# Kernel optimization log

Measured on AMD Instinct MI355X. Metric: run time of the kernel, lower is better.

## Reference

```python
import jax, jax.numpy as jnp
import numpy as np

GRID_SIZE = 128  # D = H = W
N_POINTS = 8388608


def setup_inputs() -> dict:
    key = jax.random.key(0)
    k_grid, k_coords = jax.random.split(key)
    # occupancy grid buffer: binary {0,1} values as float, shape [D, H, W]
    grid = (jax.random.uniform(k_grid, (GRID_SIZE, GRID_SIZE, GRID_SIZE)) > 0.5).astype(jnp.float32)
    # normalized [-1, 1] query coordinates, layout [..., 3] = (x, y, z)
    coords = jax.random.uniform(k_coords, (N_POINTS, 3), minval=-1.0, maxval=1.0, dtype=jnp.float32)
    return {"grid": grid, "coords": coords}


def _trilinear_sample(grid, coords):
    """torch.nn.functional.grid_sample 5D, mode='bilinear', align_corners=False,
    padding_mode='zeros'. grid: [D,H,W]; coords: [N,3] with (x,y,z) where
    x indexes W, y indexes H, z indexes D. Returns [N]."""
    D, H, W = grid.shape
    x, y, z = coords[:, 0], coords[:, 1], coords[:, 2]
    # unnormalize (align_corners=False): pixel = ((c + 1) * size - 1) / 2
    ix = ((x + 1.0) * W - 1.0) * 0.5
    iy = ((y + 1.0) * H - 1.0) * 0.5
    iz = ((z + 1.0) * D - 1.0) * 0.5

    ix0 = jnp.floor(ix)
    iy0 = jnp.floor(iy)
    iz0 = jnp.floor(iz)
    wx = ix - ix0  # fractional weights
    wy = iy - iy0
    wz = iz - iz0
    ix0 = ix0.astype(jnp.int32)
    iy0 = iy0.astype(jnp.int32)
    iz0 = iz0.astype(jnp.int32)

    def gather(zi, yi, xi):
        # zero padding: out-of-bounds corners contribute 0
        valid = ((zi >= 0) & (zi < D) & (yi >= 0) & (yi < H) & (xi >= 0) & (xi < W))
        zc = jnp.clip(zi, 0, D - 1)
        yc = jnp.clip(yi, 0, H - 1)
        xc = jnp.clip(xi, 0, W - 1)
        return jnp.where(valid, grid[zc, yc, xc], 0.0)

    out = (
        gather(iz0,     iy0,     ix0    ) * (1 - wz) * (1 - wy) * (1 - wx)
        + gather(iz0,     iy0,     ix0 + 1) * (1 - wz) * (1 - wy) * wx
        + gather(iz0,     iy0 + 1, ix0    ) * (1 - wz) * wy       * (1 - wx)
        + gather(iz0,     iy0 + 1, ix0 + 1) * (1 - wz) * wy       * wx
        + gather(iz0 + 1, iy0,     ix0    ) * wz       * (1 - wy) * (1 - wx)
        + gather(iz0 + 1, iy0,     ix0 + 1) * wz       * (1 - wy) * wx
        + gather(iz0 + 1, iy0 + 1, ix0    ) * wz       * wy       * (1 - wx)
        + gather(iz0 + 1, iy0 + 1, ix0 + 1) * wz       * wy       * wx
    )
    return out


def reference(grid, coords):
    flat = coords.reshape(-1, 3)
    return _trilinear_sample(grid, flat)
```

## Files before the change

kernel.cpp:

```cpp
#include <hip/hip_runtime.h>


typedef float fx4 __attribute__((ext_vector_type(4)));
typedef unsigned int u32;
typedef unsigned int ux4 __attribute__((ext_vector_type(4)));
typedef unsigned long long u64;

constexpr int GS = 128;
constexpr int PROW_W  = 5;
constexpr int PPLANE_W = 130 * PROW_W;
constexpr int PMASK_WORDS = 130 * PPLANE_W;
constexpr size_t PMASK_BYTES = (size_t)PMASK_WORDS * 4;

constexpr size_t MASK_BYTES = (size_t)GS * GS * GS / 8;
constexpr size_t MASK_OFF   = (PMASK_BYTES + 63) & ~(size_t)63;
constexpr size_t WS_MAIN    = MASK_OFF + MASK_BYTES;

constexpr int TD = GS + 1;
constexpr size_t TBL_BYTES = (size_t)TD * TD * TD;
constexpr size_t TBL_OFF   = MASK_OFF + MASK_BYTES;
constexpr size_t WS_FB     = TBL_OFF + TBL_BYTES;

constexpr int SLAB_ALLOC_WORDS = 46 * PPLANE_W + 1;
constexpr size_t SLAB_LDS = (size_t)SLAB_ALLOC_WORDS * 4;

__global__ __launch_bounds__(256)
void bitpack_kernel(const float* __restrict__ grid, u64* __restrict__ mask) {
    int gid = blockIdx.x * blockDim.x + threadIdx.x;
    float v = grid[gid];
    u64 m = __ballot(v != 0.0f);
    if ((threadIdx.x & 63) == 0) mask[gid >> 6] = m;
}

__global__ __launch_bounds__(256)
void padmask_kernel(const u32* __restrict__ mask32, u32* __restrict__ pmask) {
    int i = blockIdx.x * blockDim.x + threadIdx.x;
    if (i >= PMASK_WORDS) return;
    int k = i % PROW_W;
    int r = i / PROW_W;
    int py = r % 130;
    int pz = r / 130;
    int y = py - 1, z = pz - 1;
    u32 w = 0;
    if (((unsigned)y < 128u) & ((unsigned)z < 128u)) {
        const u32* vrow = mask32 + (z * 128 + y) * 4;
        u32 lo = (k >= 1) ? vrow[k - 1] : 0u;
        u32 hi = (k < 4) ? vrow[k] : 0u;
        w = (lo >> 31) | (hi << 1);
    }
    pmask[i] = w;
}

__global__ __launch_bounds__(1024, 4)
void sample_slab3(const u32* __restrict__ pmask,
                  const float* __restrict__ coords,
                  float* __restrict__ out) {
    extern __shared__ u32 lds[];
    const int tid = threadIdx.x;
    const int T = blockIdx.x * 1024 + tid;
    const fx4* c4 = (const fx4*)coords;
    fx4 q[6];
#pragma unroll
    for (int j = 0; j < 6; ++j) q[j] = c4[6 * T + j];
    const float* f = (const float*)q;

    u32 pr[8];
    float wx[8], wy[8], wz[8], o[8];
#pragma unroll
    for (int j = 0; j < 8; ++j) {
        float ix = fmaf(f[3 * j + 0], 64.0f, 63.5f);
        float iy = fmaf(f[3 * j + 1], 64.0f, 63.5f);
        float iz = fmaf(f[3 * j + 2], 64.0f, 63.5f);
        float fx = floorf(ix), fy = floorf(iy), fz = floorf(iz);
        wx[j] = ix - fx; wy[j] = iy - fy; wz[j] = iz - fz;
        int X  = (int)fx + 1;
        int Y  = (int)fy + 1;
        int PZ = (int)fz + 1;
        int k = X >> 5, p = X & 31;
        u32 R = (u32)((PZ * 130 + Y) * PROW_W + k);
        pr[j] = R | ((u32)p << 20) | ((u32)PZ << 25);
        o[j] = 0.0f;
    }

#pragma unroll 1
    for (int s = 0; s < 3; ++s) {
        const int p0 = (s == 0) ? 0 : (s == 1 ? 44 : 88);
        const int np = (s == 2) ? 42 : 46;
        const int lo = (s == 0) ? 0 : (s == 1 ? 45 : 89);
        const int hi = (s == 0) ? 44 : (s == 1 ? 88 : 128);
        __syncthreads();
        {
            const int nv = np * PPLANE_W / 4;
            const ux4* src = (const ux4*)(pmask + p0 * PPLANE_W);
            ux4* dst = (ux4*)lds;
            for (int i = tid; i < nv; i += 1024) dst[i] = src[i];
        }
        __syncthreads();
#pragma unroll
        for (int j = 0; j < 8; ++j) {
            int PZ = (int)(pr[j] >> 25);
            if ((unsigned)(PZ - lo) > (unsigned)(hi - lo)) continue;
            int p  = (int)((pr[j] >> 20) & 31u);
            int rb = (int)(pr[j] & 0xFFFFFu) - p0 * PPLANE_W;
            int rb2 = rb + PPLANE_W;
            u32 a0 = lds[rb],      a1 = lds[rb + 1];
            u32 b0 = lds[rb + 5],  b1 = lds[rb + 6];
            u32 c0 = lds[rb2],     c1 = lds[rb2 + 1];
            u32 d0 = lds[rb2 + 5], d1 = lds[rb2 + 6];
            u32 t00 = (u32)((((u64)a1 << 32) | a0) >> p) & 3u;
            u32 t01 = (u32)((((u64)b1 << 32) | b0) >> p) & 3u;
            u32 t10 = (u32)((((u64)c1 << 32) | c0) >> p) & 3u;
            u32 t11 = (u32)((((u64)d1 << 32) | d0) >> p) & 3u;
            float w = wx[j];
            float r00 = fmaf(w, (float)(t00 >> 1) - (float)(t00 & 1u), (float)(t00 & 1u));
            float r01 = fmaf(w, (float)(t01 >> 1) - (float)(t01 & 1u), (float)(t01 & 1u));
            float r10 = fmaf(w, (float)(t10 >> 1) - (float)(t10 & 1u), (float)(t10 & 1u));
            float r11 = fmaf(w, (float)(t11 >> 1) - (float)(t11 & 1u), (float)(t11 & 1u));
            float cy0 = fmaf(wy[j], r01 - r00, r00);
            float cy1 = fmaf(wy[j], r11 - r10, r10);
            o[j] = fmaf(wz[j], cy1 - cy0, cy0);
        }
    }
    fx4* o4 = (fx4*)out;
    fx4 r0 = {o[0], o[1], o[2], o[3]};
    fx4 r1 = {o[4], o[5], o[6], o[7]};
    o4[2 * T]     = r0;
    o4[2 * T + 1] = r1;
}

__device__ __forceinline__ unsigned bit_at(u64 lo, u64 hi, int xi) {
    if ((unsigned)xi >= 128u) return 0u;
    u64 w = (xi < 64) ? lo : hi;
    return (unsigned)((w >> (xi & 63)) & 1ull);
}

__global__ __launch_bounds__(256)
void table_kernel(const u64* __restrict__ mask, unsigned char* __restrict__ tbl) {
    int i = blockIdx.x * blockDim.x + threadIdx.x;
    if (i >= (int)TBL_BYTES) return;
    int x = i % TD;
    int t = i / TD;
    int y = t % TD;
    int z = t / TD;
    int x0 = x - 1;
    unsigned byte = 0u;
#pragma unroll
    for (int dz = 0; dz < 2; ++dz) {
#pragma unroll
        for (int dy = 0; dy < 2; ++dy) {
            int yi = y - 1 + dy, zi = z - 1 + dz;
            u64 lo = 0ull, hi = 0ull;
            if (((unsigned)yi < 128u) & ((unsigned)zi < 128u)) {
                int r = (zi * 128 + yi) * 2;
                lo = mask[r];
                hi = mask[r + 1];
            }
            int kk = dy * 2 + dz * 4;
            byte |= (bit_at(lo, hi, x0) << kk) | (bit_at(lo, hi, x0 + 1) << (kk + 1));
        }
    }
    tbl[i] = (unsigned char)byte;
}

__global__ __launch_bounds__(256)
void sample_packed(const unsigned char* __restrict__ tbl,
                   const float* __restrict__ coords,
                   float* __restrict__ out, int nt) {
    int t = blockIdx.x * blockDim.x + threadIdx.x;
    if (t >= nt) return;
    const fx4* c4 = (const fx4*)coords;
    fx4 q[6];
#pragma unroll
    for (int j = 0; j < 6; ++j) q[j] = c4[6 * t + j];
    const float* f = (const float*)q;
    float wxa[8], wya[8], wza[8];
    int addr[8];
#pragma unroll
    for (int i = 0; i < 8; ++i) {
        float ix = fmaf(f[3 * i + 0], 64.0f, 63.5f);
        float iy = fmaf(f[3 * i + 1], 64.0f, 63.5f);
        float iz = fmaf(f[3 * i + 2], 64.0f, 63.5f);
        float fx = floorf(ix), fy = floorf(iy), fz = floorf(iz);
        wxa[i] = ix - fx; wya[i] = iy - fy; wza[i] = iz - fz;
        int xb = (int)fx + 1, yb = (int)fy + 1, zb = (int)fz + 1;
        addr[i] = (zb * TD + yb) * TD + xb;
    }
    unsigned bytes[8];
#pragma unroll
    for (int i = 0; i < 8; ++i) bytes[i] = (unsigned)tbl[addr[i]];
    float o[8];
#pragma unroll
    for (int i = 0; i < 8; ++i) {
        unsigned byte = bytes[i];
        float wx = wxa[i], wy = wya[i], wz = wza[i];
        float v0 = (float)( byte       & 1u);
        float v1 = (float)((byte >> 1) & 1u);
        float v2 = (float)((byte >> 2) & 1u);
        float v3 = (float)((byte >> 3) & 1u);
        float v4 = (float)((byte >> 4) & 1u);
        float v5 = (float)((byte >> 5) & 1u);
        float v6 = (float)((byte >> 6) & 1u);
        float v7 = (float)((byte >> 7) & 1u);
        float c00 = v0 + wx * (v1 - v0);
        float c10 = v2 + wx * (v3 - v2);
        float c01 = v4 + wx * (v5 - v4);
        float c11 = v6 + wx * (v7 - v6);
        float c0  = c00 + wy * (c10 - c00);
        float c1  = c01 + wy * (c11 - c01);
        o[i] = c0 + wz * (c1 - c0);
    }
    fx4* o4 = (fx4*)out;
    fx4 r0 = {o[0], o[1], o[2], o[3]};
    fx4 r1 = {o[4], o[5], o[6], o[7]};
    o4[2 * t + 0] = r0;
    o4[2 * t + 1] = r1;
}

extern "C" void kernel_launch(void* const* d_in, const int* in_sizes, int n_in,
                              void* d_out, int out_size, void* d_ws, size_t ws_size,
                              hipStream_t stream) {
    const float* grid   = (const float*)d_in[0];
    const float* coords = (const float*)d_in[1];
    float* out = (float*)d_out;
    int npts = in_sizes[1] / 3;
    int vox = GS * GS * GS;

    u32* pmask = (u32*)d_ws;
    u64* mask  = (u64*)((char*)d_ws + MASK_OFF);

    (void)hipFuncSetAttribute((const void*)sample_slab3,
                              hipFuncAttributeMaxDynamicSharedMemorySize,
                              (int)SLAB_LDS);
    int nb = 0;
    hipError_t oe = hipOccupancyMaxActiveBlocksPerMultiprocessor(
        &nb, sample_slab3, 1024, SLAB_LDS);
    bool slab_ok = (oe == hipSuccess) && (nb >= 1) && (ws_size >= WS_MAIN) &&
                   (npts == 1024 * 1024 * 8);

    if (slab_ok) {
        bitpack_kernel<<<vox / 256, 256, 0, stream>>>(grid, mask);
        padmask_kernel<<<(PMASK_WORDS + 255) / 256, 256, 0, stream>>>((const u32*)mask, pmask);
        sample_slab3<<<1024, 1024, SLAB_LDS, stream>>>(pmask, coords, out);
    } else if (ws_size >= WS_FB) {
        unsigned char* tbl = (unsigned char*)d_ws + TBL_OFF;
        bitpack_kernel<<<vox / 256, 256, 0, stream>>>(grid, mask);
        table_kernel<<<(int)((TBL_BYTES + 255) / 256), 256, 0, stream>>>(mask, tbl);
        int nt = npts / 8;
        sample_packed<<<(nt + 255) / 256, 256, 0, stream>>>(tbl, coords, out, nt);
    }
}
```

Before: 194.7 us.

## Sample from unpadded bitmask in two LDS slabs, dropping padmask kernel

Removes the padded-mask kernel and samples directly from the raw 128^3 bitmask. The grid is now staged into LDS in two z-slabs of about 130KB each instead of three padded slabs. Out-of-bounds corners are handled with per-point validity masks, an x-flip trick at the left edge, and alignbit for the bit extraction. This cuts one kernel launch, one slab pass and its barriers, in exchange for more per-point mask arithmetic and more LDS per block, which may lower occupancy.

```diff
diff --git a/kernel.cpp b/kernel.cpp
--- a/kernel.cpp
+++ b/kernel.cpp
@@ -7,22 +7,14 @@
 typedef unsigned long long u64;
 
 constexpr int GS = 128;
-constexpr int PROW_W  = 5;
-constexpr int PPLANE_W = 130 * PROW_W;
-constexpr int PMASK_WORDS = 130 * PPLANE_W;
-constexpr size_t PMASK_BYTES = (size_t)PMASK_WORDS * 4;
-
 constexpr size_t MASK_BYTES = (size_t)GS * GS * GS / 8;
-constexpr size_t MASK_OFF   = (PMASK_BYTES + 63) & ~(size_t)63;
-constexpr size_t WS_MAIN    = MASK_OFF + MASK_BYTES;
+constexpr int SLAB_WORDS = 33281;
+constexpr size_t SLAB_LDS = (size_t)SLAB_WORDS * 4;
 
 constexpr int TD = GS + 1;
 constexpr size_t TBL_BYTES = (size_t)TD * TD * TD;
-constexpr size_t TBL_OFF   = MASK_OFF + MASK_BYTES;
+constexpr size_t TBL_OFF   = (MASK_BYTES + 63) & ~(size_t)63;
 constexpr size_t WS_FB     = TBL_OFF + TBL_BYTES;
-
-constexpr int SLAB_ALLOC_WORDS = 46 * PPLANE_W + 1;
-constexpr size_t SLAB_LDS = (size_t)SLAB_ALLOC_WORDS * 4;
 
 __global__ __launch_bounds__(256)
 void bitpack_kernel(const float* __restrict__ grid, u64* __restrict__ mask) {
@@ -32,29 +24,10 @@
     if ((threadIdx.x & 63) == 0) mask[gid >> 6] = m;
 }
 
-__global__ __launch_bounds__(256)
-void padmask_kernel(const u32* __restrict__ mask32, u32* __restrict__ pmask) {
-    int i = blockIdx.x * blockDim.x + threadIdx.x;
-    if (i >= PMASK_WORDS) return;
-    int k = i % PROW_W;
-    int r = i / PROW_W;
-    int py = r % 130;
-    int pz = r / 130;
-    int y = py - 1, z = pz - 1;
-    u32 w = 0;
-    if (((unsigned)y < 128u) & ((unsigned)z < 128u)) {
-        const u32* vrow = mask32 + (z * 128 + y) * 4;
-        u32 lo = (k >= 1) ? vrow[k - 1] : 0u;
-        u32 hi = (k < 4) ? vrow[k] : 0u;
-        w = (lo >> 31) | (hi << 1);
-    }
-    pmask[i] = w;
-}
-
 __global__ __launch_bounds__(1024, 4)
-void sample_slab3(const u32* __restrict__ pmask,
-                  const float* __restrict__ coords,
-                  float* __restrict__ out) {
+void sample_2p(const u32* __restrict__ mask32,
+               const float* __restrict__ coords,
+               float* __restrict__ out) {
     extern __shared__ u32 lds[];
     const int tid = threadIdx.x;
     const int T = blockIdx.x * 1024 + tid;
@@ -64,7 +37,8 @@
     for (int j = 0; j < 6; ++j) q[j] = c4[6 * T + j];
     const float* f = (const float*)q;
 
-    u32 pr[8];
+    u32 pack1[8];
+    u32 AM = 0;
     float wx[8], wy[8], wz[8], o[8];
 #pragma unroll
     for (int j = 0; j < 8; ++j) {
@@ -72,50 +46,71 @@
         float iy = fmaf(f[3 * j + 1], 64.0f, 63.5f);
         float iz = fmaf(f[3 * j + 2], 64.0f, 63.5f);
         float fx = floorf(ix), fy = floorf(iy), fz = floorf(iz);
-        wx[j] = ix - fx; wy[j] = iy - fy; wz[j] = iz - fz;
-        int X  = (int)fx + 1;
-        int Y  = (int)fy + 1;
-        int PZ = (int)fz + 1;
-        int k = X >> 5, p = X & 31;
-        u32 R = (u32)((PZ * 130 + Y) * PROW_W + k);
-        pr[j] = R | ((u32)p << 20) | ((u32)PZ << 25);
+        float w0 = ix - fx;
+        wy[j] = iy - fy; wz[j] = iz - fz;
+        int x0 = (int)fx, y0 = (int)fy, z0 = (int)fz;
+        int zb = z0 + 1;
+        bool flip = (x0 < 0);
+        wx[j] = flip ? 1.0f - w0 : w0;
+        int xc = flip ? 0 : x0;
+        int sft = xc & 31;
+        u32 xm = ((u32)x0 <= 126u) ? 3u : 1u;
+        u32 vy0 = (u32)(y0 >= 0);
+        u32 vy1 = (u32)((u32)y0 <= 126u);
+        u32 a0 = vy0 ? xm : 0u;
+        u32 a1 = vy1 ? xm : 0u;
+        u32 am = a0 | (a1 << 2);
+        u32 dyf = vy0 & vy1;
+        int y0c = y0 < 0 ? 0 : y0;
+        int z0c = z0 < 0 ? 0 : z0;
+        u32 RA = (u32)(((z0c << 7) + y0c) * 4 + (xc >> 5));
+        pack1[j] = RA | ((u32)sft << 16) | ((u32)zb << 21) | (dyf << 29);
+        AM |= am << (4 * j);
         o[j] = 0.0f;
     }
 
 #pragma unroll 1
-    for (int s = 0; s < 3; ++s) {
-        const int p0 = (s == 0) ? 0 : (s == 1 ? 44 : 88);
-        const int np = (s == 2) ? 42 : 46;
-        const int lo = (s == 0) ? 0 : (s == 1 ? 45 : 89);
-        const int hi = (s == 0) ? 44 : (s == 1 ? 88 : 128);
+    for (int s = 0; s < 2; ++s) {
+        const int base_w = s ? 32256 : 0;
+        const int nv4    = s ? 8320 : 8192;
         __syncthreads();
         {
-            const int nv = np * PPLANE_W / 4;
-            const ux4* src = (const ux4*)(pmask + p0 * PPLANE_W);
+            const ux4* src = (const ux4*)(mask32 + base_w);
             ux4* dst = (ux4*)lds;
-            for (int i = tid; i < nv; i += 1024) dst[i] = src[i];
+            for (int i = tid; i < nv4; i += 1024) dst[i] = src[i];
+            if (s && tid == 0) lds[33280] = 0;
         }
         __syncthreads();
 #pragma unroll
         for (int j = 0; j < 8; ++j) {
-            int PZ = (int)(pr[j] >> 25);
-            if ((unsigned)(PZ - lo) > (unsigned)(hi - lo)) continue;
-            int p  = (int)((pr[j] >> 20) & 31u);
-            int rb = (int)(pr[j] & 0xFFFFFu) - p0 * PPLANE_W;
-            int rb2 = rb + PPLANE_W;
-            u32 a0 = lds[rb],      a1 = lds[rb + 1];
-            u32 b0 = lds[rb + 5],  b1 = lds[rb + 6];
-            u32 c0 = lds[rb2],     c1 = lds[rb2 + 1];
-            u32 d0 = lds[rb2 + 5], d1 = lds[rb2 + 6];
-            u32 t00 = (u32)((((u64)a1 << 32) | a0) >> p) & 3u;
-            u32 t01 = (u32)((((u64)b1 << 32) | b0) >> p) & 3u;
-            u32 t10 = (u32)((((u64)c1 << 32) | c0) >> p) & 3u;
-            u32 t11 = (u32)((((u64)d1 << 32) | d0) >> p) & 3u;
+            u32 p1 = pack1[j];
+            int zb = (int)((p1 >> 21) & 0xFF);
+            if ((zb < 64) != (s == 0)) continue;
+            int la  = (int)(p1 & 0xFFFF) - base_w;
+            int sft = (int)((p1 >> 16) & 31);
+            int dyw = (int)((p1 >> 27) & 4);
+            bool edge = s ? (zb == 128) : (zb == 0);
+            int dz = edge ? 0 : 512;
+            u32 amv = (AM >> (4 * j)) & 15u;
+            u32 glo = amv, ghi = amv;
+            if (s) ghi = edge ? 0u : amv;
+            else   glo = edge ? 0u : amv;
+            int l0 = la, l1 = la + dyw, l2 = la + dz, l3 = la + dz + dyw;
+            u32 w00 = lds[l0], w01 = lds[l0 + 1];
+            u32 w10 = lds[l1], w11 = lds[l1 + 1];
+            u32 w20 = lds[l2], w21 = lds[l2 + 1];
+            u32 w30 = lds[l3], w31 = lds[l3 + 1];
+            u32 t0 = __builtin_amdgcn_alignbit(w01, w00, (u32)sft) & (glo & 3u);
+            u32 t1 = __builtin_amdgcn_alignbit(w11, w10, (u32)sft) & ((glo >> 2) & 3u);
+            u32 t2 = __builtin_amdgcn_alignbit(w21, w20, (u32)sft) & (ghi & 3u);
+            u32 t3 = __builtin_amdgcn_alignbit(w31, w30, (u32)sft) & ((ghi >> 2) & 3u);
             float w = wx[j];
-            float r00 = fmaf(w, (float)(t00 >> 1) - (float)(t00 & 1u), (float)(t00 & 1u));
-            float r01 = fmaf(w, (float)(t01 >> 1) - (float)(t01 & 1u), (float)(t01 & 1u));
-            float r10 = fmaf(w, (float)(t10 >> 1) - (float)(t10 & 1u), (float)(t10 & 1u));
-            float r11 = fmaf(w, (float)(t11 >> 1) - (float)(t11 & 1u), (float)(t11 & 1u));
+            int b0 = (int)(t0 & 1u), b1 = (int)(t1 & 1u);
+            int b2 = (int)(t2 & 1u), b3 = (int)(t3 & 1u);
+            float r00 = fmaf(w, (float)((int)(t0 >> 1) - b0), (float)b0);
+            float r01 = fmaf(w, (float)((int)(t1 >> 1) - b1), (float)b1);
+            float r10 = fmaf(w, (float)((int)(t2 >> 1) - b2), (float)b2);
+            float r11 = fmaf(w, (float)((int)(t3 >> 1) - b3), (float)b3);
             float cy0 = fmaf(wy[j], r01 - r00, r00);
             float cy1 = fmaf(wy[j], r11 - r10, r10);
             o[j] = fmaf(wz[j], cy1 - cy0, cy0);
@@ -225,22 +220,20 @@
     int npts = in_sizes[1] / 3;
     int vox = GS * GS * GS;
 
-    u32* pmask = (u32*)d_ws;
-    u64* mask  = (u64*)((char*)d_ws + MASK_OFF);
-
-    (void)hipFuncSetAttribute((const void*)sample_slab3,
+    u64* mask = (u64*)d_ws;
+
+    (void)hipFuncSetAttribute((const void*)sample_2p,
                               hipFuncAttributeMaxDynamicSharedMemorySize,
                               (int)SLAB_LDS);
     int nb = 0;
     hipError_t oe = hipOccupancyMaxActiveBlocksPerMultiprocessor(
-        &nb, sample_slab3, 1024, SLAB_LDS);
-    bool slab_ok = (oe == hipSuccess) && (nb >= 1) && (ws_size >= WS_MAIN) &&
-                   (npts == 1024 * 1024 * 8);
+        &nb, sample_2p, 1024, SLAB_LDS);
+    bool slab_ok = (oe == hipSuccess) && (nb >= 1) && (ws_size >= MASK_BYTES) &&
+                   (npts == 1024 * 8192);
 
     if (slab_ok) {
         bitpack_kernel<<<vox / 256, 256, 0, stream>>>(grid, mask);
-        padmask_kernel<<<(PMASK_WORDS + 255) / 256, 256, 0, stream>>>((const u32*)mask, pmask);
-        sample_slab3<<<1024, 1024, SLAB_LDS, stream>>>(pmask, coords, out);
+        sample_2p<<<1024, 1024, SLAB_LDS, stream>>>((const u32*)mask, coords, out);
     } else if (ws_size >= WS_FB) {
         unsigned char* tbl = (unsigned char*)d_ws + TBL_OFF;
         bitpack_kernel<<<vox / 256, 256, 0, stream>>>(grid, mask);
```

After: 194.4 us. Within noise of the previous version (-0.2%).
